# Kernel tuning notes

Measured on AMD Instinct MI355X. Metric: run time of the kernel, lower is better.

## Reference

```python
import jax, jax.numpy as jnp
import numpy as np

B, S, H, NH = 4, 1024, 3072, 32
D = H // NH  # head_dim = 96
I = 8192
EPS = 1e-5


def _layernorm(x, g, b):
    mu = jnp.mean(x, axis=-1, keepdims=True)
    var = jnp.mean(jnp.square(x - mu), axis=-1, keepdims=True)
    return (x - mu) * jax.lax.rsqrt(var + EPS) * g + b


def _gelu_tanh(x):
    c = np.sqrt(2.0 / np.pi).astype(np.float32)
    return 0.5 * x * (1.0 + jnp.tanh(c * (x + 0.044715 * x * x * x)))


def setup_inputs() -> dict:
    key = jax.random.key(0)
    ks = jax.random.split(key, 8)
    s = 0.02
    causal = jnp.tril(jnp.ones((S, S), dtype=bool))[None, None]  # [1,1,S,S]
    return {
        "hidden_states": jax.random.normal(ks[0], (B, S, H), jnp.float32),
        "attention_mask": causal,
        "Wq": jax.random.normal(ks[1], (H, H), jnp.float32) * s,
        "Wk": jax.random.normal(ks[2], (H, H), jnp.float32) * s,
        "Wv": jax.random.normal(ks[3], (H, H), jnp.float32) * s,
        "Wo": jax.random.normal(ks[4], (H, H), jnp.float32) * s,
        "bo": jnp.zeros((H,), jnp.float32),
        "ln1_g": jnp.ones((H,), jnp.float32),
        "ln1_b": jnp.zeros((H,), jnp.float32),
        "ln2_g": jnp.ones((H,), jnp.float32),
        "ln2_b": jnp.zeros((H,), jnp.float32),
        "W1": jax.random.normal(ks[5], (H, I), jnp.float32) * s,
        "b1": jnp.zeros((I,), jnp.float32),
        "W2": jax.random.normal(ks[6], (I, H), jnp.float32) * s,
        "b2": jnp.zeros((H,), jnp.float32),
    }


def reference(hidden_states, attention_mask, Wq, Wk, Wv, Wo, bo,
              ln1_g, ln1_b, ln2_g, ln2_b, W1, b1, W2, b2):
    x = hidden_states
    # --- pre-attention LN ---
    h = _layernorm(x, ln1_g, ln1_b)
    # --- attention ---
    q = (h @ Wq).reshape(B, S, NH, D).transpose(0, 2, 1, 3)  # [B,NH,S,D]
    k = (h @ Wk).reshape(B, S, NH, D).transpose(0, 2, 1, 3)
    v = (h @ Wv).reshape(B, S, NH, D).transpose(0, 2, 1, 3)
    scale = 1.0 / np.sqrt(D).astype(np.float32)
    scores = jnp.einsum("bhqd,bhkd->bhqk", q, k) * scale  # [B,NH,S,S]
    scores = jnp.where(attention_mask, scores, jnp.float32(-1e9))
    probs = jax.nn.softmax(scores, axis=-1)
    ctx = jnp.einsum("bhqk,bhkd->bhqd", probs, v)  # [B,NH,S,D]
    ctx = ctx.transpose(0, 2, 1, 3).reshape(B, S, H)
    attn_out = ctx @ Wo + bo
    x = x + attn_out
    # --- MLP ---
    h = _layernorm(x, ln2_g, ln2_b)
    mlp = _gelu_tanh(h @ W1 + b1) @ W2 + b2
    return x + mlp
```

## Files before the change

kernel.cpp:

```cpp
#include <hip/hip_runtime.h>
#include <hip/hip_bf16.h>

typedef __attribute__((ext_vector_type(8))) short short8;
typedef __attribute__((ext_vector_type(4))) float f32x4;
typedef __hip_bfloat16 bf16;

#define GLDS16(gp, lp) __builtin_amdgcn_global_load_lds( \
    (const __attribute__((address_space(1))) void*)(gp), \
    (__attribute__((address_space(3))) void*)(lp), 16, 0, 0)

__device__ __forceinline__ short f2bf(float f){
  bf16 h = __float2bfloat16(f);
  return *reinterpret_cast<short*>(&h);
}

__global__ __launch_bounds__(256) void wconv_kernel(
    const float* __restrict__ W, bf16* __restrict__ Wt, int K, int N)
{
  __shared__ float tile[32][33];
  const int tk = blockIdx.y * 32, tn = blockIdx.x * 32;
  const int t = threadIdx.x;
#pragma unroll
  for (int i = 0; i < 4; ++i){
    int idx = i*256 + t, r = idx >> 5, c = idx & 31;
    tile[r][c] = W[(size_t)(tk + r) * N + (tn + c)];
  }
  __syncthreads();
#pragma unroll
  for (int i = 0; i < 4; ++i){
    int idx = i*256 + t, r = idx >> 5, c = idx & 31;
    Wt[(size_t)(tn + r) * K + (tk + c)] = __float2bfloat16(tile[c][r]);
  }
}

__global__ __launch_bounds__(256) void ln_kernel(
    const float* __restrict__ x, const float* __restrict__ g,
    const float* __restrict__ bb, bf16* __restrict__ out)
{
  const int row = blockIdx.x, t = threadIdx.x;
  const float4* xr = (const float4*)(x + (size_t)row * 3072);
  float4 v[3];
  float s = 0.f, s2 = 0.f;
#pragma unroll
  for (int i = 0; i < 3; ++i){
    v[i] = xr[i*256 + t];
    s  += v[i].x + v[i].y + v[i].z + v[i].w;
    s2 += v[i].x*v[i].x + v[i].y*v[i].y + v[i].z*v[i].z + v[i].w*v[i].w;
  }
#pragma unroll
  for (int d = 1; d < 64; d <<= 1){ s += __shfl_xor(s, d); s2 += __shfl_xor(s2, d); }
  __shared__ float red[2][4];
  const int w = t >> 6, lane = t & 63;
  if (lane == 0){ red[0][w] = s; red[1][w] = s2; }
  __syncthreads();
  s  = red[0][0] + red[0][1] + red[0][2] + red[0][3];
  s2 = red[1][0] + red[1][1] + red[1][2] + red[1][3];
  const float mu = s * (1.f/3072.f);
  const float rstd = rsqrtf(s2 * (1.f/3072.f) - mu*mu + 1e-5f);
  const float4* g4 = (const float4*)g;
  const float4* b4 = (const float4*)bb;
  uint2* ov = (uint2*)(out + (size_t)row * 3072);
#pragma unroll
  for (int i = 0; i < 3; ++i){
    const int c = i*256 + t;
    float4 gv = g4[c], bv = b4[c], xv = v[i];
    float o0 = (xv.x - mu) * rstd * gv.x + bv.x;
    float o1 = (xv.y - mu) * rstd * gv.y + bv.y;
    float o2 = (xv.z - mu) * rstd * gv.z + bv.z;
    float o3 = (xv.w - mu) * rstd * gv.w + bv.w;
    uint2 pk;
    pk.x = (unsigned)(unsigned short)f2bf(o0) | ((unsigned)(unsigned short)f2bf(o1) << 16);
    pk.y = (unsigned)(unsigned short)f2bf(o2) | ((unsigned)(unsigned short)f2bf(o3) << 16);
    ov[c] = pk;
  }
}

template<int EPI>
__global__ __launch_bounds__(512, 2) void gemm8_kernel(
    const bf16* __restrict__ A, const bf16* __restrict__ Bt,
    const float* __restrict__ bias, const float* __restrict__ res,
    void* __restrict__ outp, int M, int N, int K)
{
  __shared__ __align__(16) char lds[131072];
  const int NT = K >> 6;
  const int nbx = N >> 8;
  const int nwg = nbx * (M >> 8);
  const int cpx = nwg >> 3;
  const int bid = blockIdx.x;
  const int lg = (bid & 7) * cpx + (bid >> 3);
  const int by = lg / nbx, bx = lg - by * nbx;
  const int m0 = by << 8, n0 = bx << 8;

  const int tid = threadIdx.x;
  const int lane = tid & 63, wid = tid >> 6;
  const int wm = wid >> 2, wn = wid & 3;
  const int l15 = lane & 15, lhi = lane >> 4;

  const int row0 = tid >> 2;
  const int ce = ((tid & 3) ^ ((tid >> 3) & 3)) * 8;
  const bf16* pA0 = A  + (size_t)(m0 + row0) * K + ce;
  const bf16* pA1 = pA0 + (size_t)128 * K;
  const bf16* pB0 = Bt + (size_t)(n0 + row0) * K + ce;
  const bf16* pB1 = pB0 + (size_t)128 * K;

  auto stage = [&](int s){
    if (s < (NT << 2)){
      const int kt = s >> 2, idx = s & 3;
      const int koff = (kt << 6) + ((idx >> 1) << 5);
      const bf16* g0 = (idx & 1) ? pB0 : pA0;
      const bf16* g1 = (idx & 1) ? pB1 : pA1;
      char* d = lds + ((kt & 1) << 16) + (idx << 14) + (tid << 4);
      GLDS16(g0 + koff, d);
      GLDS16(g1 + koff, d + 8192);
    }
  };

  f32x4 acc[8][4];
#pragma unroll
  for (int i = 0; i < 8; ++i)
#pragma unroll
    for (int j = 0; j < 4; ++j) acc[i][j] = (f32x4){0.f,0.f,0.f,0.f};

  const int swz = (lhi ^ ((l15 >> 1) & 3)) << 4;
  const int aoff = (wm*128 + l15)*64 + swz;
  const int boff = 16384 + (wn*64 + l15)*64 + swz;

  stage(0); stage(1); stage(2); stage(3);
  asm volatile("s_waitcnt vmcnt(4)" ::: "memory");
  __builtin_amdgcn_s_barrier();

  for (int t = 0; t < NT; ++t){
    const char* Lb = lds + ((t & 1) << 16);
    short8 af[8], b0, b1;

#pragma unroll
    for (int mi = 0; mi < 8; ++mi) af[mi] = *(const short8*)(Lb + aoff + mi*1024);
    b0 = *(const short8*)(Lb + boff);
    b1 = *(const short8*)(Lb + boff + 1024);
    stage((t << 2) + 4);
    __builtin_amdgcn_s_barrier();
    __builtin_amdgcn_s_setprio(1);
#pragma unroll
    for (int mi = 0; mi < 8; ++mi){
      acc[mi][0] = __builtin_amdgcn_mfma_f32_16x16x32_bf16(af[mi], b0, acc[mi][0], 0,0,0);
      acc[mi][1] = __builtin_amdgcn_mfma_f32_16x16x32_bf16(af[mi], b1, acc[mi][1], 0,0,0);
    }
    __builtin_amdgcn_s_setprio(0);
    __builtin_amdgcn_s_barrier();

    b0 = *(const short8*)(Lb + boff + 2048);
    b1 = *(const short8*)(Lb + boff + 3072);
    stage((t << 2) + 5);
    __builtin_amdgcn_s_barrier();
    __builtin_amdgcn_s_setprio(1);
#pragma unroll
    for (int mi = 0; mi < 8; ++mi){
      acc[mi][2] = __builtin_amdgcn_mfma_f32_16x16x32_bf16(af[mi], b0, acc[mi][2], 0,0,0);
      acc[mi][3] = __builtin_amdgcn_mfma_f32_16x16x32_bf16(af[mi], b1, acc[mi][3], 0,0,0);
    }
    __builtin_amdgcn_s_setprio(0);
    asm volatile("s_waitcnt vmcnt(4)" ::: "memory");
    __builtin_amdgcn_s_barrier();

#pragma unroll
    for (int mi = 0; mi < 8; ++mi) af[mi] = *(const short8*)(Lb + 32768 + aoff + mi*1024);
    b0 = *(const short8*)(Lb + 32768 + boff);
    b1 = *(const short8*)(Lb + 32768 + boff + 1024);
    stage((t << 2) + 6);
    __builtin_amdgcn_s_barrier();
    __builtin_amdgcn_s_setprio(1);
#pragma unroll
    for (int mi = 0; mi < 8; ++mi){
      acc[mi][0] = __builtin_amdgcn_mfma_f32_16x16x32_bf16(af[mi], b0, acc[mi][0], 0,0,0);
      acc[mi][1] = __builtin_amdgcn_mfma_f32_16x16x32_bf16(af[mi], b1, acc[mi][1], 0,0,0);
    }
    __builtin_amdgcn_s_setprio(0);
    __builtin_amdgcn_s_barrier();

    b0 = *(const short8*)(Lb + 32768 + boff + 2048);
    b1 = *(const short8*)(Lb + 32768 + boff + 3072);
    stage((t << 2) + 7);
    __builtin_amdgcn_s_barrier();
    __builtin_amdgcn_s_setprio(1);
#pragma unroll
    for (int mi = 0; mi < 8; ++mi){
      acc[mi][2] = __builtin_amdgcn_mfma_f32_16x16x32_bf16(af[mi], b0, acc[mi][2], 0,0,0);
      acc[mi][3] = __builtin_amdgcn_mfma_f32_16x16x32_bf16(af[mi], b1, acc[mi][3], 0,0,0);
    }
    __builtin_amdgcn_s_setprio(0);
    asm volatile("s_waitcnt vmcnt(4)" ::: "memory");
    __builtin_amdgcn_s_barrier();
  }

  const int rb = m0 + wm*128 + (lhi << 2);
  const int cb0 = n0 + wn*64 + l15;
#pragma unroll
  for (int mi = 0; mi < 8; ++mi){
#pragma unroll
    for (int ni = 0; ni < 4; ++ni){
      const int col = cb0 + ni*16;
#pragma unroll
      for (int r = 0; r < 4; ++r){
        const int row = rb + mi*16 + r;
        float vv = acc[mi][ni][r];
        if constexpr (EPI == 0){
          const int cbuf = col / 3072;
          const int cl = col - cbuf*3072;
          ((bf16*)outp)[(size_t)cbuf*M*3072 + (size_t)row*3072 + cl] = __float2bfloat16(vv);
        } else if constexpr (EPI == 1){
          ((float*)outp)[(size_t)row*N + col] = vv + bias[col] + res[(size_t)row*N + col];
        } else {
          float xx = vv + bias[col];
          float y = 0.7978845608f*(xx + 0.044715f*xx*xx*xx);
          float e = exp2f(fminf(y, 15.f) * 2.885390082f);
          ((bf16*)outp)[(size_t)row*N + col] = __float2bfloat16(xx * e / (e + 1.f));
        }
      }
    }
  }
}

__global__ __launch_bounds__(256) void vt_kernel(
    const bf16* __restrict__ V, bf16* __restrict__ VT)
{
  const int bh = blockIdx.x, st = blockIdx.y;
  const int b = bh >> 5, h = bh & 31;
  const int t = threadIdx.x;
  __shared__ __align__(16) short tile[96][72];
  const int s0 = st*64;
  const short* src = (const short*)V + (size_t)(b*1024 + s0)*3072 + h*96;
#pragma unroll
  for (int i = 0; i < 3; ++i){
    int c = t + i*256;
    int s = c/12, dc = c - s*12;
    short8 v8 = *(const short8*)(src + (size_t)s*3072 + dc*8);
#pragma unroll
    for (int e = 0; e < 8; ++e) tile[dc*8+e][s] = v8[e];
  }
  __syncthreads();
  short* dst = (short*)VT + ((size_t)bh*96)*1024 + s0;
#pragma unroll
  for (int i = 0; i < 3; ++i){
    int c = t + i*256;
    int d = c >> 3, kc = c & 7;
    short8 v8 = *(const short8*)(&tile[0][0] + d*72 + kc*8);
    *(short8*)(dst + (size_t)d*1024 + kc*8) = v8;
  }
}

__global__ __launch_bounds__(256, 4) void attn_kernel(
    const bf16* __restrict__ Q, const bf16* __restrict__ Kg,
    const bf16* __restrict__ VT, bf16* __restrict__ O)
{
  const int bh = blockIdx.x;
  const int yp = blockIdx.y;
  const int b = bh >> 5, h = bh & 31;
  const int t = threadIdx.x;
  const int lane = t & 63, w = t >> 6;
  const size_t RS = 3072;
  const size_t base = (size_t)(b * 1024) * RS + (size_t)h * 96;
  const short* VTh = (const short*)VT + (size_t)bh * 96 * 1024;

  __shared__ __align__(16) bf16 Ks[64*128];
  __shared__ __align__(16) bf16 Vt[96*64];
  __shared__ __align__(16) bf16 Ps[4][16][72];

  char* KsB = (char*)Ks;
  char* VtB = (char*)Vt;
  const short* PsW = (const short*)&Ps[w][0][0];
  const float sc = 0.1020620726f * 1.44269504089f;
  const int l15 = lane & 15, lhi = lane >> 4;

#pragma unroll
  for (int sel = 0; sel < 2; ++sel){
    const int qt = sel ? (15 - yp) : yp;
    const int q0 = qt*64 + w*16;

    short8 aq[3];
    {
      const short* qp = (const short*)Q + base + (size_t)(q0 + l15) * RS + (lhi << 3);
#pragma unroll
      for (int ks = 0; ks < 3; ++ks) aq[ks] = *(const short8*)(qp + ks*32);
    }
    f32x4 acc[6];
#pragma unroll
    for (int i = 0; i < 6; ++i) acc[i] = (f32x4){0.f,0.f,0.f,0.f};
    float mrow[4] = {-3e38f,-3e38f,-3e38f,-3e38f};
    float lrow[4] = {0.f,0.f,0.f,0.f};

    for (int kt = 0; kt <= qt; ++kt){
      const int kv0 = kt*64;
      __syncthreads();
      {
        short8 kr[4], vr[3];
#pragma unroll
        for (int i = 0; i < 4; ++i){
          int c = t + i*256, kv = c >> 4, dc = c & 15;
          kr[i] = *(const short8*)((const short*)Kg + base + (size_t)(kv0 + kv)*RS + dc*8);
        }
#pragma unroll
        for (int i = 0; i < 3; ++i){
          int c = t + i*256, d = c >> 3, kvc = c & 7;
          vr[i] = *(const short8*)(VTh + (size_t)d*1024 + kv0 + kvc*8);
        }
#pragma unroll
        for (int i = 0; i < 4; ++i){
          int c = t + i*256, kv = c >> 4, dc = c & 15;
          *(short8*)(KsB + kv*256 + ((dc ^ (kv & 7)) << 4)) = kr[i];
        }
#pragma unroll
        for (int i = 0; i < 3; ++i){
          int c = t + i*256, d = c >> 3, kvc = c & 7;
          *(short8*)(VtB + d*128 + ((kvc ^ (d & 7)) << 4)) = vr[i];
        }
      }
      __syncthreads();

      float sv[4][4];
      const bool diag = (kt == qt);
#pragma unroll
      for (int ct = 0; ct < 4; ++ct){
        const int kvl = ct*16 + l15;
        f32x4 s4 = (f32x4){0.f,0.f,0.f,0.f};
#pragma unroll
        for (int ks = 0; ks < 3; ++ks){
          short8 bk = *(const short8*)(KsB + kvl*256 + (((ks*4 + lhi) ^ (kvl & 7)) << 4));
          s4 = __builtin_amdgcn_mfma_f32_16x16x32_bf16(aq[ks], bk, s4, 0,0,0);
        }
#pragma unroll
        for (int r = 0; r < 4; ++r){
          float vvl = s4[r] * sc;
          if (diag){
            int kvg = kv0 + kvl;
            int qg  = q0 + (lhi << 2) + r;
            if (kvg > qg) vvl = -3e38f;
          }
          sv[ct][r] = vvl;
        }
      }

      float alpha[4];
#pragma unroll
      for (int r = 0; r < 4; ++r){
        float m = fmaxf(fmaxf(sv[0][r], sv[1][r]), fmaxf(sv[2][r], sv[3][r]));
#pragma unroll
        for (int dd = 1; dd < 16; dd <<= 1) m = fmaxf(m, __shfl_xor(m, dd));
        float mn = fmaxf(mrow[r], m);
        alpha[r] = exp2f(mrow[r] - mn);
        mrow[r] = mn;
        float rs = 0.f;
#pragma unroll
        for (int ct = 0; ct < 4; ++ct){
          float p = exp2f(sv[ct][r] - mn);
          sv[ct][r] = p;
          rs += p;
        }
#pragma unroll
        for (int dd = 1; dd < 16; dd <<= 1) rs += __shfl_xor(rs, dd);
        lrow[r] = lrow[r]*alpha[r] + rs;
      }
#pragma unroll
      for (int i = 0; i < 6; ++i)
#pragma unroll
        for (int r = 0; r < 4; ++r) acc[i][r] *= alpha[r];

#pragma unroll
      for (int ct = 0; ct < 4; ++ct)
#pragma unroll
        for (int r = 0; r < 4; ++r)
          Ps[w][(lhi << 2) + r][ct*16 + l15] = __float2bfloat16(sv[ct][r]);

#pragma unroll
      for (int ks2 = 0; ks2 < 2; ++ks2){
        short8 pa = *(const short8*)(PsW + l15*72 + ks2*32 + (lhi << 3));
#pragma unroll
        for (int dt = 0; dt < 6; ++dt){
          const int dl = dt*16 + l15;
          short8 vbf = *(const short8*)(VtB + dl*128 + (((ks2*4 + lhi) ^ (dl & 7)) << 4));
          acc[dt] = __builtin_amdgcn_mfma_f32_16x16x32_bf16(pa, vbf, acc[dt], 0,0,0);
        }
      }
    }

    bf16* Ob = (bf16*)O + base + (size_t)q0 * RS;
#pragma unroll
    for (int dt = 0; dt < 6; ++dt){
#pragma unroll
      for (int r = 0; r < 4; ++r){
        float vvl = acc[dt][r] / lrow[r];
        Ob[(size_t)((lhi << 2) + r) * RS + dt*16 + l15] = __float2bfloat16(vvl);
      }
    }
  }
}

extern "C" void kernel_launch(void* const* d_in, const int* in_sizes, int n_in,
                              void* d_out, int out_size, void* d_ws, size_t ws_size,
                              hipStream_t stream)
{
  (void)in_sizes; (void)n_in; (void)out_size; (void)ws_size;
  const float* x_in = (const float*)d_in[0];
  const float* Wq   = (const float*)d_in[2];
  const float* Wk   = (const float*)d_in[3];
  const float* Wv   = (const float*)d_in[4];
  const float* Wo   = (const float*)d_in[5];
  const float* bo   = (const float*)d_in[6];
  const float* ln1g = (const float*)d_in[7];
  const float* ln1b = (const float*)d_in[8];
  const float* ln2g = (const float*)d_in[9];
  const float* ln2b = (const float*)d_in[10];
  const float* W1   = (const float*)d_in[11];
  const float* b1   = (const float*)d_in[12];
  const float* W2   = (const float*)d_in[13];
  const float* b2   = (const float*)d_in[14];

  char* ws = (char*)d_ws;
  size_t off = 0;
  auto alloc = [&](size_t bytes) -> char* {
    char* p = ws + off; off += (bytes + 255) & ~(size_t)255; return p;
  };
  const size_t H = 3072, I = 8192, M = 4096;
  bf16* Wqt = (bf16*)alloc(H*H*2);
  bf16* Wkt = (bf16*)alloc(H*H*2);
  bf16* Wvt = (bf16*)alloc(H*H*2);
  bf16* Wot = (bf16*)alloc(H*H*2);
  bf16* W1t = (bf16*)alloc(H*I*2);
  bf16* W2t = (bf16*)alloc(H*I*2);
  bf16* hb  = (bf16*)alloc(M*H*2);
  bf16* qb  = (bf16*)alloc(M*H*2);
  bf16* kb  = (bf16*)alloc(M*H*2);
  bf16* vb  = (bf16*)alloc(M*H*2);
  bf16* ctx = (bf16*)alloc(M*H*2);
  float* x2 = (float*)d_out;
  bf16* h2  = hb;
  bf16* VT  = hb;
  bf16* act = qb;
  (void)kb; (void)vb;

  wconv_kernel<<<dim3(96, 96),  256, 0, stream>>>(Wq, Wqt, 3072, 3072);
  wconv_kernel<<<dim3(96, 96),  256, 0, stream>>>(Wk, Wkt, 3072, 3072);
  wconv_kernel<<<dim3(96, 96),  256, 0, stream>>>(Wv, Wvt, 3072, 3072);
  wconv_kernel<<<dim3(96, 96),  256, 0, stream>>>(Wo, Wot, 3072, 3072);
  wconv_kernel<<<dim3(256, 96), 256, 0, stream>>>(W1, W1t, 3072, 8192);
  wconv_kernel<<<dim3(96, 256), 256, 0, stream>>>(W2, W2t, 8192, 3072);

  ln_kernel<<<4096, 256, 0, stream>>>(x_in, ln1g, ln1b, hb);

  gemm8_kernel<0><<<576, 512, 0, stream>>>(hb, Wqt, nullptr, nullptr, qb, 4096, 9216, 3072);

  vt_kernel<<<dim3(128, 16), 256, 0, stream>>>(vb, VT);

  attn_kernel<<<dim3(128, 8), 256, 0, stream>>>(qb, kb, VT, ctx);

  gemm8_kernel<1><<<192, 512, 0, stream>>>(ctx, Wot, bo, x_in, x2, 4096, 3072, 3072);

  ln_kernel<<<4096, 256, 0, stream>>>(x2, ln2g, ln2b, h2);

  gemm8_kernel<2><<<512, 512, 0, stream>>>(h2, W1t, b1, nullptr, act, 4096, 8192, 3072);

  gemm8_kernel<1><<<192, 512, 0, stream>>>(act, W2t, b2, x2, (float*)d_out, 4096, 3072, 8192);
}
```

Baseline: 1.044 ms.

## Restructure GEMM main loop into register double-buffered 4x4 MFMA quadrants

Restructures the inner GEMM loop so each phase computes a 4x4 block of MFMAs from register fragments loaded in the previous phase. LDS reads for the next quadrant are issued before the current MFMAs, with explicit lgkmcnt waits and sched_barriers to overlap LDS latency with matrix math. The next tile's first fragments are prefetched from the other buffer at the end of each iteration. The cost is more live registers and tighter hand-tuned wait counts, which risks register pressure or hazards if the counts are wrong.

```diff
diff --git a/kernel.cpp b/kernel.cpp
--- a/kernel.cpp
+++ b/kernel.cpp
@@ -125,70 +125,76 @@
   const int aoff = (wm*128 + l15)*64 + swz;
   const int boff = 16384 + (wn*64 + l15)*64 + swz;
 
+  short8 A0[4], A1[4], B0[4], B1[4];
+  auto dsrA = [&](short8* dst, int buf, int ks, int hi){
+#pragma unroll
+    for (int i = 0; i < 4; ++i)
+      dst[i] = *(const short8*)(lds + (buf << 16) + (ks << 15) + aoff + hi*4096 + i*1024);
+  };
+  auto dsrB = [&](short8* dst, int buf, int ks){
+#pragma unroll
+    for (int i = 0; i < 4; ++i)
+      dst[i] = *(const short8*)(lds + (buf << 16) + (ks << 15) + boff + i*1024);
+  };
+  auto mf16 = [&](const short8* Ar, const short8* Br, int r0){
+#pragma unroll
+    for (int mi = 0; mi < 4; ++mi)
+#pragma unroll
+      for (int ni = 0; ni < 4; ++ni)
+        acc[r0 + mi][ni] = __builtin_amdgcn_mfma_f32_16x16x32_bf16(Ar[mi], Br[ni], acc[r0 + mi][ni], 0,0,0);
+  };
+
   stage(0); stage(1); stage(2); stage(3);
   asm volatile("s_waitcnt vmcnt(4)" ::: "memory");
   __builtin_amdgcn_s_barrier();
+  dsrA(A0, 0, 0, 0);
+  dsrB(B0, 0, 0);
 
   for (int t = 0; t < NT; ++t){
-    const char* Lb = lds + ((t & 1) << 16);
-    short8 af[8], b0, b1;
-
-#pragma unroll
-    for (int mi = 0; mi < 8; ++mi) af[mi] = *(const short8*)(Lb + aoff + mi*1024);
-    b0 = *(const short8*)(Lb + boff);
-    b1 = *(const short8*)(Lb + boff + 1024);
+    const int buf = t & 1, nbuf = buf ^ 1;
+
+    dsrA(A1, buf, 0, 1);
     stage((t << 2) + 4);
     __builtin_amdgcn_s_barrier();
+    asm volatile("s_waitcnt lgkmcnt(4)" ::: "memory");
+    __builtin_amdgcn_sched_barrier(0);
     __builtin_amdgcn_s_setprio(1);
-#pragma unroll
-    for (int mi = 0; mi < 8; ++mi){
-      acc[mi][0] = __builtin_amdgcn_mfma_f32_16x16x32_bf16(af[mi], b0, acc[mi][0], 0,0,0);
-      acc[mi][1] = __builtin_amdgcn_mfma_f32_16x16x32_bf16(af[mi], b1, acc[mi][1], 0,0,0);
-    }
+    mf16(A0, B0, 0);
     __builtin_amdgcn_s_setprio(0);
-    __builtin_amdgcn_s_barrier();
-
-    b0 = *(const short8*)(Lb + boff + 2048);
-    b1 = *(const short8*)(Lb + boff + 3072);
+    asm volatile("s_waitcnt vmcnt(2)" ::: "memory");
+    __builtin_amdgcn_s_barrier();
+
+    dsrA(A0, buf, 1, 0);
+    dsrB(B1, buf, 1);
     stage((t << 2) + 5);
     __builtin_amdgcn_s_barrier();
+    asm volatile("s_waitcnt lgkmcnt(8)" ::: "memory");
+    __builtin_amdgcn_sched_barrier(0);
     __builtin_amdgcn_s_setprio(1);
-#pragma unroll
-    for (int mi = 0; mi < 8; ++mi){
-      acc[mi][2] = __builtin_amdgcn_mfma_f32_16x16x32_bf16(af[mi], b0, acc[mi][2], 0,0,0);
-      acc[mi][3] = __builtin_amdgcn_mfma_f32_16x16x32_bf16(af[mi], b1, acc[mi][3], 0,0,0);
-    }
+    mf16(A1, B0, 4);
     __builtin_amdgcn_s_setprio(0);
-    asm volatile("s_waitcnt vmcnt(4)" ::: "memory");
-    __builtin_amdgcn_s_barrier();
-
-#pragma unroll
-    for (int mi = 0; mi < 8; ++mi) af[mi] = *(const short8*)(Lb + 32768 + aoff + mi*1024);
-    b0 = *(const short8*)(Lb + 32768 + boff);
-    b1 = *(const short8*)(Lb + 32768 + boff + 1024);
+    __builtin_amdgcn_s_barrier();
+
+    dsrA(A1, buf, 1, 1);
     stage((t << 2) + 6);
     __builtin_amdgcn_s_barrier();
+    asm volatile("s_waitcnt lgkmcnt(4)" ::: "memory");
+    __builtin_amdgcn_sched_barrier(0);
     __builtin_amdgcn_s_setprio(1);
-#pragma unroll
-    for (int mi = 0; mi < 8; ++mi){
-      acc[mi][0] = __builtin_amdgcn_mfma_f32_16x16x32_bf16(af[mi], b0, acc[mi][0], 0,0,0);
-      acc[mi][1] = __builtin_amdgcn_mfma_f32_16x16x32_bf16(af[mi], b1, acc[mi][1], 0,0,0);
-    }
+    mf16(A0, B1, 0);
     __builtin_amdgcn_s_setprio(0);
-    __builtin_amdgcn_s_barrier();
-
-    b0 = *(const short8*)(Lb + 32768 + boff + 2048);
-    b1 = *(const short8*)(Lb + 32768 + boff + 3072);
+    asm volatile("s_waitcnt vmcnt(2)" ::: "memory");
+    __builtin_amdgcn_s_barrier();
+
+    dsrA(A0, nbuf, 0, 0);
+    dsrB(B0, nbuf, 0);
     stage((t << 2) + 7);
     __builtin_amdgcn_s_barrier();
+    asm volatile("s_waitcnt lgkmcnt(8)" ::: "memory");
+    __builtin_amdgcn_sched_barrier(0);
     __builtin_amdgcn_s_setprio(1);
-#pragma unroll
-    for (int mi = 0; mi < 8; ++mi){
-      acc[mi][2] = __builtin_amdgcn_mfma_f32_16x16x32_bf16(af[mi], b0, acc[mi][2], 0,0,0);
-      acc[mi][3] = __builtin_amdgcn_mfma_f32_16x16x32_bf16(af[mi], b1, acc[mi][3], 0,0,0);
-    }
+    mf16(A1, B1, 4);
     __builtin_amdgcn_s_setprio(0);
-    asm volatile("s_waitcnt vmcnt(4)" ::: "memory");
     __builtin_amdgcn_s_barrier();
   }
 
```

New measurement: 1.070 ms. 2.5% more time.

## Restructure GEMM mainloop into 4-stage ring with one barrier per k-step

Applied to the files above, without the earlier changes.

Replaces the two-buffer, four-sub-stage pipeline (K=64 per iteration with four barriers) with a four-slot LDS ring of K=32 tiles, prefetching three tiles ahead. Each iteration does a single waitcnt plus barrier, then issues the A and B prefetches interleaved with two groups of 16 MFMAs. The aim is to cut barrier count and synchronisation stalls while keeping more loads in flight. The risk is that the vmcnt(8) accounting across the ring slots is wrong, and that the deeper prefetch raises register and LDS pressure.

```diff
diff --git a/kernel.cpp b/kernel.cpp
--- a/kernel.cpp
+++ b/kernel.cpp
@@ -82,7 +82,7 @@
     void* __restrict__ outp, int M, int N, int K)
 {
   __shared__ __align__(16) char lds[131072];
-  const int NT = K >> 6;
+  const int NT = K >> 5;
   const int nbx = N >> 8;
   const int nwg = nbx * (M >> 8);
   const int cpx = nwg >> 3;
@@ -103,15 +103,18 @@
   const bf16* pB0 = Bt + (size_t)(n0 + row0) * K + ce;
   const bf16* pB1 = pB0 + (size_t)128 * K;
 
-  auto stage = [&](int s){
-    if (s < (NT << 2)){
-      const int kt = s >> 2, idx = s & 3;
-      const int koff = (kt << 6) + ((idx >> 1) << 5);
-      const bf16* g0 = (idx & 1) ? pB0 : pA0;
-      const bf16* g1 = (idx & 1) ? pB1 : pA1;
-      char* d = lds + ((kt & 1) << 16) + (idx << 14) + (tid << 4);
-      GLDS16(g0 + koff, d);
-      GLDS16(g1 + koff, d + 8192);
+  auto stageA = [&](int u){
+    if (u < NT){
+      char* d = lds + ((u & 3) << 15) + (tid << 4);
+      GLDS16(pA0 + ((size_t)u << 5), d);
+      GLDS16(pA1 + ((size_t)u << 5), d + 8192);
+    }
+  };
+  auto stageB = [&](int u){
+    if (u < NT){
+      char* d = lds + ((u & 3) << 15) + 16384 + (tid << 4);
+      GLDS16(pB0 + ((size_t)u << 5), d);
+      GLDS16(pB1 + ((size_t)u << 5), d + 8192);
     }
   };
 
@@ -125,71 +128,38 @@
   const int aoff = (wm*128 + l15)*64 + swz;
   const int boff = 16384 + (wn*64 + l15)*64 + swz;
 
-  stage(0); stage(1); stage(2); stage(3);
-  asm volatile("s_waitcnt vmcnt(4)" ::: "memory");
-  __builtin_amdgcn_s_barrier();
+  stageA(0); stageB(0); stageA(1); stageB(1); stageA(2); stageB(2);
 
   for (int t = 0; t < NT; ++t){
-    const char* Lb = lds + ((t & 1) << 16);
-    short8 af[8], b0, b1;
-
-#pragma unroll
-    for (int mi = 0; mi < 8; ++mi) af[mi] = *(const short8*)(Lb + aoff + mi*1024);
-    b0 = *(const short8*)(Lb + boff);
-    b1 = *(const short8*)(Lb + boff + 1024);
-    stage((t << 2) + 4);
+    const char* Lb = lds + ((t & 3) << 15);
+    asm volatile("s_waitcnt vmcnt(8)" ::: "memory");
     __builtin_amdgcn_s_barrier();
+    __builtin_amdgcn_sched_barrier(0);
+
+    stageA(t + 3);
+    short8 a[4], b[4];
+#pragma unroll
+    for (int i = 0; i < 4; ++i) a[i] = *(const short8*)(Lb + aoff + i*1024);
+#pragma unroll
+    for (int i = 0; i < 4; ++i) b[i] = *(const short8*)(Lb + boff + i*1024);
     __builtin_amdgcn_s_setprio(1);
 #pragma unroll
-    for (int mi = 0; mi < 8; ++mi){
-      acc[mi][0] = __builtin_amdgcn_mfma_f32_16x16x32_bf16(af[mi], b0, acc[mi][0], 0,0,0);
-      acc[mi][1] = __builtin_amdgcn_mfma_f32_16x16x32_bf16(af[mi], b1, acc[mi][1], 0,0,0);
-    }
+    for (int mi = 0; mi < 4; ++mi)
+#pragma unroll
+      for (int ni = 0; ni < 4; ++ni)
+        acc[mi][ni] = __builtin_amdgcn_mfma_f32_16x16x32_bf16(a[mi], b[ni], acc[mi][ni], 0,0,0);
     __builtin_amdgcn_s_setprio(0);
-    __builtin_amdgcn_s_barrier();
-
-    b0 = *(const short8*)(Lb + boff + 2048);
-    b1 = *(const short8*)(Lb + boff + 3072);
-    stage((t << 2) + 5);
-    __builtin_amdgcn_s_barrier();
+
+    stageB(t + 3);
+#pragma unroll
+    for (int i = 0; i < 4; ++i) a[i] = *(const short8*)(Lb + aoff + (4+i)*1024);
     __builtin_amdgcn_s_setprio(1);
 #pragma unroll
-    for (int mi = 0; mi < 8; ++mi){
-      acc[mi][2] = __builtin_amdgcn_mfma_f32_16x16x32_bf16(af[mi], b0, acc[mi][2], 0,0,0);
-      acc[mi][3] = __builtin_amdgcn_mfma_f32_16x16x32_bf16(af[mi], b1, acc[mi][3], 0,0,0);
-    }
+    for (int mi = 0; mi < 4; ++mi)
+#pragma unroll
+      for (int ni = 0; ni < 4; ++ni)
+        acc[4+mi][ni] = __builtin_amdgcn_mfma_f32_16x16x32_bf16(a[mi], b[ni], acc[4+mi][ni], 0,0,0);
     __builtin_amdgcn_s_setprio(0);
-    asm volatile("s_waitcnt vmcnt(4)" ::: "memory");
-    __builtin_amdgcn_s_barrier();
-
-#pragma unroll
-    for (int mi = 0; mi < 8; ++mi) af[mi] = *(const short8*)(Lb + 32768 + aoff + mi*1024);
-    b0 = *(const short8*)(Lb + 32768 + boff);
-    b1 = *(const short8*)(Lb + 32768 + boff + 1024);
-    stage((t << 2) + 6);
-    __builtin_amdgcn_s_barrier();
-    __builtin_amdgcn_s_setprio(1);
-#pragma unroll
-    for (int mi = 0; mi < 8; ++mi){
-      acc[mi][0] = __builtin_amdgcn_mfma_f32_16x16x32_bf16(af[mi], b0, acc[mi][0], 0,0,0);
-      acc[mi][1] = __builtin_amdgcn_mfma_f32_16x16x32_bf16(af[mi], b1, acc[mi][1], 0,0,0);
-    }
-    __builtin_amdgcn_s_setprio(0);
-    __builtin_amdgcn_s_barrier();
-
-    b0 = *(const short8*)(Lb + 32768 + boff + 2048);
-    b1 = *(const short8*)(Lb + 32768 + boff + 3072);
-    stage((t << 2) + 7);
-    __builtin_amdgcn_s_barrier();
-    __builtin_amdgcn_s_setprio(1);
-#pragma unroll
-    for (int mi = 0; mi < 8; ++mi){
-      acc[mi][2] = __builtin_amdgcn_mfma_f32_16x16x32_bf16(af[mi], b0, acc[mi][2], 0,0,0);
-      acc[mi][3] = __builtin_amdgcn_mfma_f32_16x16x32_bf16(af[mi], b1, acc[mi][3], 0,0,0);
-    }
-    __builtin_amdgcn_s_setprio(0);
-    asm volatile("s_waitcnt vmcnt(4)" ::: "memory");
-    __builtin_amdgcn_s_barrier();
   }
 
   const int rb = m0 + wm*128 + (lhi << 2);
```

New measurement: 1.025 ms. No clear change (-1.9%).
